# Optimization experiments

Measured on AMD Instinct MI355X. Metric: run time of the kernel, lower is better.

## Reference

```python
import jax, jax.numpy as jnp
import numpy as np


def conv3d(x, w, b):
    # x: [B,C,T,H,W], w: [O,I,3,3,3], padding=1, stride=1
    y = jax.lax.conv_general_dilated(
        x, w, window_strides=(1, 1, 1), padding=((1, 1), (1, 1), (1, 1)),
        dimension_numbers=('NCDHW', 'OIDHW', 'NCDHW'))
    return y + b[None, :, None, None, None]


def deform_conv3d(x, offsets, w, b):
    # Deformable 3D conv, kernel 3, pad 1, stride 1, no modulation mask.
    # offsets: [B, 81, T, H, W] -> [B, 27, 3(t,h,w), T, H, W]
    B, Cin, T, H, W = x.shape
    nk = 27
    off = offsets.reshape(B, nk, 3, T, H, W)
    r = jnp.arange(3, dtype=x.dtype) - 1.0  # kernel taps {-1,0,1}
    kt, kh, kw = jnp.meshgrid(r, r, r, indexing='ij')
    koff = jnp.stack([kt.ravel(), kh.ravel(), kw.ravel()], axis=-1)  # [27,3]
    bt = jnp.arange(T, dtype=x.dtype)[:, None, None]
    bh = jnp.arange(H, dtype=x.dtype)[None, :, None]
    bw = jnp.arange(W, dtype=x.dtype)[None, None, :]
    base = jnp.stack(jnp.broadcast_arrays(bt, bh, bw), axis=0)  # [3,T,H,W]
    pos = base[None, None] + koff[None, :, :, None, None, None] + off  # [B,27,3,T,H,W]
    pt, ph, pw = pos[:, :, 0], pos[:, :, 1], pos[:, :, 2]
    ft, fh, fw = jnp.floor(pt), jnp.floor(ph), jnp.floor(pw)
    at, ah, aw = pt - ft, ph - fh, pw - fw
    it, ih, iw = ft.astype(jnp.int32), fh.astype(jnp.int32), fw.astype(jnp.int32)
    N = T * H * W
    xf = x.reshape(B, Cin, N)
    gather = jax.vmap(lambda xb, lb: xb[:, lb])  # ([Cin,N],[27,N])->[Cin,27,N]
    acc = jnp.zeros((B, Cin, nk, N), dtype=x.dtype)
    # trilinear interpolation: accumulate 8 corners, zero outside bounds
    for dt in (0, 1):
        tti = it + dt
        wt = (1.0 - at) if dt == 0 else at
        vt = (tti >= 0) & (tti < T)
        tc = jnp.clip(tti, 0, T - 1)
        for dh in (0, 1):
            hhi = ih + dh
            wh = (1.0 - ah) if dh == 0 else ah
            vh = (hhi >= 0) & (hhi < H)
            hc = jnp.clip(hhi, 0, H - 1)
            for dw in (0, 1):
                wwi = iw + dw
                ww = (1.0 - aw) if dw == 0 else aw
                vw = (wwi >= 0) & (wwi < W)
                wc = jnp.clip(wwi, 0, W - 1)
                wgt = (wt * wh * ww) * (vt & vh & vw).astype(x.dtype)  # [B,27,T,H,W]
                lin = (tc * H + hc) * W + wc  # [B,27,T,H,W]
                g = gather(xf, lin.reshape(B, nk, N))  # [B,Cin,27,N]
                acc = acc + wgt.reshape(B, 1, nk, N) * g
    out = jnp.einsum('oik,bikn->bon', w.reshape(w.shape[0], Cin, nk), acc)
    out = out + b[None, :, None]
    return out.reshape(B, w.shape[0], T, H, W)


def setup_inputs() -> dict:
    key = jax.random.key(0)
    ks = jax.random.split(key, 12)
    B, Cin, Cout, mdim = 1, 256, 256, 256
    T, H, W = 8, 24, 24

    def winit(k, shape):
        fan_in = int(np.prod(shape[1:]))
        return jax.random.normal(k, shape, jnp.float32) / np.float32(np.sqrt(fan_in))

    return {
        'x': jax.random.normal(ks[0], (B, Cin, T, H, W), jnp.float32),
        'l1_w': winit(ks[1], (mdim, Cin, 3, 3, 3)),
        'l1_b': jnp.zeros((mdim,), jnp.float32),
        'l2_w': winit(ks[2], (mdim, mdim, 3, 3, 3)),
        'l2_b': jnp.zeros((mdim,), jnp.float32),
        'l3_w': winit(ks[3], (mdim, mdim, 3, 3, 3)),
        'l3_b': jnp.zeros((mdim,), jnp.float32),
        'def_w': winit(ks[4], (81, mdim, 3, 3, 3)) * 0.1,  # keep offsets small
        'def_b': jnp.zeros((81,), jnp.float32),
        'c3d_w': winit(ks[5], (Cout, Cin, 3, 3, 3)),
        'c3d_b': jnp.zeros((Cout,), jnp.float32),
    }


def reference(x, l1_w, l1_b, l2_w, l2_b, l3_w, l3_b, def_w, def_b, c3d_w, c3d_b):
    h = jax.nn.relu(conv3d(x, l1_w, l1_b))
    h = jax.nn.relu(conv3d(h, l2_w, l2_b))
    h = jax.nn.relu(conv3d(h, l3_w, l3_b))
    offsets = conv3d(h, def_w, def_b)  # [B,81,T,H,W]
    return deform_conv3d(x, offsets, c3d_w, c3d_b)
```

## Files before the change

kernel.cpp:

```cpp
#include <hip/hip_runtime.h>

#define TT 8
#define HH 24
#define WW 24
#define NN 4608
#define CIN 256
#define N3 6760
#define KDIM 6912
#define BK 64
#define KTILES 108
#define NSPLIT 9
#define KT_PER 12

typedef short short8 __attribute__((ext_vector_type(8)));
typedef short short4v __attribute__((ext_vector_type(4)));
typedef float f32x4  __attribute__((ext_vector_type(4)));
typedef int   i32x4  __attribute__((ext_vector_type(4)));
typedef unsigned int u32x4 __attribute__((ext_vector_type(4)));

#define MFMA16 __builtin_amdgcn_mfma_f32_16x16x32_bf16

__device__ __forceinline__ short f2bf(float f) {
    unsigned u = __float_as_uint(f);
    unsigned r = u + 0x7fffu + ((u >> 16) & 1u);
    return (short)(r >> 16);
}
__device__ __forceinline__ float bf2f(short s) {
    return __uint_as_float(((unsigned)(unsigned short)s) << 16);
}

__device__ __forceinline__ int n3_of(int n) {
    int t = n / (HH * WW), r = n % (HH * WW), h = r / WW, w = r % WW;
    return ((t + 1) * 26 + (h + 1)) * 26 + (w + 1);
}

__device__ __forceinline__ void gload16(const void* gsrc, void* lds) {
    __builtin_amdgcn_global_load_lds(
        (const __attribute__((address_space(1))) void*)gsrc,
        (__attribute__((address_space(3))) void*)lds, 16, 0, 0);
}

__global__ __launch_bounds__(256) void prep_k(
    const float* __restrict__ x,
    const float* __restrict__ w1, const float* __restrict__ w2,
    const float* __restrict__ w3, const float* __restrict__ wc,
    const float* __restrict__ wd,
    short* __restrict__ d1, short* __restrict__ d2,
    short* __restrict__ d3, short* __restrict__ dc, short* __restrict__ dd,
    short* __restrict__ xbf3, short* __restrict__ h1b)
{
    __shared__ char smem[27648];
    const int sel = blockIdx.y;

    if (sel < 5) {
        if (blockIdx.x >= 256) return;
        const int o = blockIdx.x, ci = threadIdx.x;
        const float* w; short* dst; int Cout = 256;
        if      (sel == 0) { w = w1; dst = d1; }
        else if (sel == 1) { w = w2; dst = d2; }
        else if (sel == 2) { w = w3; dst = d3; }
        else if (sel == 3) { w = wc; dst = dc; }
        else               { w = wd; dst = dd; Cout = 81; if (o >= 128) return; }
        float* buf = (float*)smem;
        if (o < Cout) {
            const float* src = w + (size_t)o * KDIM;
            #pragma unroll
            for (int j = 0; j < 27; ++j)
                buf[j * 256 + ci] = src[j * 256 + ci];
        }
        __syncthreads();
        const int row = o & 127, y = o >> 7;
        #pragma unroll
        for (int k = 0; k < 27; ++k) {
            int K = k * 256 + ci;
            int kt = K >> 6, kk = K & 63;
            int slot = (kk >> 3) ^ (row & 7), e = kk & 7;
            size_t idx = ((size_t)(y * KTILES + kt)) * 8192 + row * 64 + slot * 8 + e;
            float v = (o < Cout) ? buf[ci * 27 + k] : 0.f;
            dst[idx] = f2bf(v);
        }
    } else if (sel == 5) {
        float (*T)[65] = (float(*)[65])smem;
        const int bx = blockIdx.x;
        const int n0 = (bx % 72) * 64, ci0 = (bx / 72) * 64;
        const int lane = threadIdx.x & 63, wave = threadIdx.x >> 6;
        #pragma unroll
        for (int j = 0; j < 16; ++j) {
            int ci_l = wave * 16 + j;
            T[ci_l][lane] = x[(size_t)(ci0 + ci_l) * NN + n0 + lane];
        }
        __syncthreads();
        #pragma unroll
        for (int j = 0; j < 16; ++j) {
            int n_l = wave * 16 + j;
            xbf3[(size_t)n3_of(n0 + n_l) * 256 + ci0 + lane] = f2bf(T[lane][n_l]);
        }
    } else {
        const int tid = threadIdx.x;
        for (int r = blockIdx.x * 27; r < min((int)(blockIdx.x * 27 + 27), N3); ++r) {
            int t3 = r / 676, rem = r % 676, h3 = rem / 26, w3 = rem % 26;
            bool interior = (t3 >= 1 && t3 <= 8 && h3 >= 1 && h3 <= 24 && w3 >= 1 && w3 <= 24);
            if (!interior && tid < 128) {
                ((unsigned*)(xbf3 + (size_t)r * 256))[tid] = 0;
                ((unsigned*)(h1b  + (size_t)r * 256))[tid] = 0;
                ((unsigned*)(h1b + 1730560 + (size_t)r * 256))[tid] = 0;
                ((unsigned*)(h1b + 3461120 + (size_t)r * 256))[tid] = 0;
            }
        }
    }
}

__global__ __launch_bounds__(256) void sample_k(
    const short* __restrict__ xbf3, const short* __restrict__ Poff,
    const float* __restrict__ dfb, short* __restrict__ S)
{
    __shared__ char recs[64 * 64];
    const int k = blockIdx.y, n0 = blockIdx.x * 64;
    const int tid = threadIdx.x;

    if (tid < 64) {
        const int n = n0 + tid;
        const int t = n / (HH * WW), r = n % (HH * WW), h = r / WW, w2 = r % WW;
        const int ki = k / 9, kj = (k % 9) / 3, kl = k % 3;
        float po[3];
        #pragma unroll
        for (int d = 0; d < 3; ++d) {
            const int ch = k * 3 + d;
            float a = 0.f;
            #pragma unroll
            for (int s = 0; s < NSPLIT; ++s)
                a += bf2f(Poff[((size_t)(s * 128 + ch)) * NN + n]);
            po[d] = a + dfb[ch];
        }
        const float pt = (float)(t  + ki - 1) + po[0];
        const float ph = (float)(h  + kj - 1) + po[1];
        const float pw = (float)(w2 + kl - 1) + po[2];
        const float ft = floorf(pt), fh = floorf(ph), fw = floorf(pw);
        const float at = pt - ft, ah = ph - fh, aw = pw - fw;
        const int it = (int)ft, ih = (int)fh, iw = (int)fw;
        i32x4 idx[2]; f32x4 wgt[2];
        #pragma unroll
        for (int dt = 0; dt < 2; ++dt)
        #pragma unroll
        for (int dh = 0; dh < 2; ++dh)
        #pragma unroll
        for (int dw = 0; dw < 2; ++dw) {
            const int c = (dt * 2 + dh) * 2 + dw;
            const int ti = it + dt, hi = ih + dh, wi = iw + dw;
            const bool v = (ti >= 0) && (ti < TT) && (hi >= 0) && (hi < HH) && (wi >= 0) && (wi < WW);
            float wv = (dt ? at : 1.f - at) * (dh ? ah : 1.f - ah) * (dw ? aw : 1.f - aw);
            const int tc = min(max(ti, 0), TT - 1), hc = min(max(hi, 0), HH - 1), wc = min(max(wi, 0), WW - 1);
            const int r3 = ((tc + 1) * 26 + (hc + 1)) * 26 + (wc + 1);
            idx[c >> 2][c & 3] = r3 * 512;
            wgt[c >> 2][c & 3] = v ? wv : 0.f;
        }
        char* rec = &recs[tid * 64];
        *(i32x4*)(rec)      = idx[0];
        *(i32x4*)(rec + 16) = idx[1];
        *(f32x4*)(rec + 32) = wgt[0];
        *(f32x4*)(rec + 48) = wgt[1];
    }
    __syncthreads();

    const int lane = tid & 63, wave = tid >> 6;
    const int half = lane >> 5, lch = lane & 31;
    const char* xb = (const char*)xbf3 + lch * 16;
    short* Sk = S + (size_t)k * NN * 256 + lch * 8;

    for (int i = 0; i < 16; i += 4) {
        const int na = wave * 16 + i + half;
        const int nb = na + 2;
        const char* ra = &recs[na * 64];
        const char* rb = &recs[nb * 64];
        const i32x4 ia0 = *(const i32x4*)(ra);
        const i32x4 ia1 = *(const i32x4*)(ra + 16);
        const f32x4 wa0 = *(const f32x4*)(ra + 32);
        const f32x4 wa1 = *(const f32x4*)(ra + 48);
        const i32x4 ib0 = *(const i32x4*)(rb);
        const i32x4 ib1 = *(const i32x4*)(rb + 16);
        const f32x4 wb0 = *(const f32x4*)(rb + 32);
        const f32x4 wb1 = *(const f32x4*)(rb + 48);

        u32x4 ga[8], gb[8];
        #pragma unroll
        for (int c = 0; c < 4; ++c) {
            ga[c]     = *(const u32x4*)(xb + ia0[c]);
            ga[c + 4] = *(const u32x4*)(xb + ia1[c]);
            gb[c]     = *(const u32x4*)(xb + ib0[c]);
            gb[c + 4] = *(const u32x4*)(xb + ib1[c]);
        }

        float sa[8] = {}, sb[8] = {};
        #pragma unroll
        for (int c = 0; c < 8; ++c) {
            const float va = (c < 4) ? wa0[c & 3] : wa1[c & 3];
            const float vb = (c < 4) ? wb0[c & 3] : wb1[c & 3];
            #pragma unroll
            for (int j = 0; j < 4; ++j) {
                sa[2*j]   = fmaf(va, __uint_as_float(ga[c][j] << 16),         sa[2*j]);
                sa[2*j+1] = fmaf(va, __uint_as_float(ga[c][j] & 0xffff0000u), sa[2*j+1]);
                sb[2*j]   = fmaf(vb, __uint_as_float(gb[c][j] << 16),         sb[2*j]);
                sb[2*j+1] = fmaf(vb, __uint_as_float(gb[c][j] & 0xffff0000u), sb[2*j+1]);
            }
        }
        short8 oa, ob;
        #pragma unroll
        for (int m = 0; m < 8; ++m) { oa[m] = f2bf(sa[m]); ob[m] = f2bf(sb[m]); }
        *(short8*)(Sk + (size_t)(n0 + na) * 256) = oa;
        *(short8*)(Sk + (size_t)(n0 + nb) * 256) = ob;
    }
}

template<int CP>
__global__ __launch_bounds__(256, 3) void gemm_conv_sk(
    const short* __restrict__ src,
    const short* __restrict__ wrb_sw,
    short* __restrict__ P)
{
    __shared__ short Ap[8192];
    __shared__ short Bw[8192];
    const int tid = threadIdx.x;
    const int l = tid & 63, w = tid >> 6;
    const int n0 = blockIdx.x * 128, co0 = blockIdx.y * 128, split = blockIdx.z;
    const int wr = w >> 1, wc = w & 1;
    const int lm = l & 15, lq = l >> 4;
    const int rswz = (lm & 7) << 3;
    const int kt0 = split * KT_PER;

    const int colA = 8 * ((l & 7) ^ ((l >> 3) & 7));
    int r3[4];
    #pragma unroll
    for (int j = 0; j < 4; ++j)
        r3[j] = n3_of(n0 + w * 32 + j * 8 + (l >> 3));
    const short* bbase = wrb_sw + ((size_t)blockIdx.y * KTILES) * 8192 + (w * 4) * 512 + l * 8;

    f32x4 acc[4][4] = {};

    for (int i = 0; i < KT_PER; ++i) {
        const int kt = kt0 + i;
        const int k = kt >> 2, ci0 = (kt & 3) * 64;
        const int dt = k / 9 - 1, dh = (k % 9) / 3 - 1, dw = k % 3 - 1;
        const int d3 = (dt * 26 + dh) * 26 + dw;
        #pragma unroll
        for (int j = 0; j < 4; ++j)
            gload16(src + (size_t)(r3[j] + d3) * 256 + ci0 + colA, &Ap[(w * 4 + j) * 512]);
        const short* b = bbase + (size_t)kt * 8192;
        #pragma unroll
        for (int j = 0; j < 4; ++j)
            gload16(b + j * 512, &Bw[(w * 4 + j) * 512]);
        __syncthreads();
        #pragma unroll
        for (int ks = 0; ks < 2; ++ks) {
            const int c = (ks * 32 + lq * 8) ^ rswz;
            short8 a[4], bf[4];
            #pragma unroll
            for (int m = 0; m < 4; ++m)
                a[m] = *(const short8*)&Ap[(wr * 64 + m * 16 + lm) * 64 + c];
            #pragma unroll
            for (int nb = 0; nb < 4; ++nb)
                bf[nb] = *(const short8*)&Bw[(wc * 64 + nb * 16 + lm) * 64 + c];
            #pragma unroll
            for (int m = 0; m < 4; ++m)
            #pragma unroll
            for (int nb = 0; nb < 4; ++nb)
                acc[m][nb] = MFMA16(a[m], bf[nb], acc[m][nb], 0, 0, 0);
        }
        __syncthreads();
    }
    #pragma unroll
    for (int m = 0; m < 4; ++m)
    #pragma unroll
    for (int nb = 0; nb < 4; ++nb) {
        int co = co0 + wc * 64 + nb * 16 + lm;
        int n = n0 + wr * 64 + m * 16 + lq * 4;
        short4v o;
        #pragma unroll
        for (int j = 0; j < 4; ++j) o[j] = f2bf(acc[m][nb][j]);
        *(short4v*)(P + ((size_t)split * CP + co) * NN + n) = o;
    }
}

__global__ __launch_bounds__(256, 3) void gemm_deform_sk(
    const short* __restrict__ S,
    const short* __restrict__ wrb_sw,
    short* __restrict__ P)
{
    __shared__ short Ap[8192];
    __shared__ short Bw[8192];
    const int tid = threadIdx.x;
    const int l = tid & 63, w = tid >> 6;
    const int n0 = blockIdx.x * 128, co0 = blockIdx.y * 128, split = blockIdx.z;
    const int wr = w >> 1, wc = w & 1;
    const int lm = l & 15, lq = l >> 4;
    const int rswz = (lm & 7) << 3;
    const int kt0 = split * KT_PER;

    const int colA = 8 * ((l & 7) ^ ((l >> 3) & 7));
    int rA[4];
    #pragma unroll
    for (int j = 0; j < 4; ++j)
        rA[j] = n0 + w * 32 + j * 8 + (l >> 3);
    const short* bbase = wrb_sw + ((size_t)blockIdx.y * KTILES) * 8192 + (w * 4) * 512 + l * 8;

    f32x4 acc[4][4] = {};

    for (int i = 0; i < KT_PER; ++i) {
        const int kt = kt0 + i;
        const int k = kt >> 2, ci0 = (kt & 3) * 64;
        #pragma unroll
        for (int j = 0; j < 4; ++j)
            gload16(S + ((size_t)k * NN + rA[j]) * 256 + ci0 + colA, &Ap[(w * 4 + j) * 512]);
        const short* b = bbase + (size_t)kt * 8192;
        #pragma unroll
        for (int j = 0; j < 4; ++j)
            gload16(b + j * 512, &Bw[(w * 4 + j) * 512]);
        __syncthreads();
        #pragma unroll
        for (int ks = 0; ks < 2; ++ks) {
            const int c = (ks * 32 + lq * 8) ^ rswz;
            short8 a[4], bf[4];
            #pragma unroll
            for (int m = 0; m < 4; ++m)
                a[m] = *(const short8*)&Ap[(wr * 64 + m * 16 + lm) * 64 + c];
            #pragma unroll
            for (int nb = 0; nb < 4; ++nb)
                bf[nb] = *(const short8*)&Bw[(wc * 64 + nb * 16 + lm) * 64 + c];
            #pragma unroll
            for (int m = 0; m < 4; ++m)
            #pragma unroll
            for (int nb = 0; nb < 4; ++nb)
                acc[m][nb] = MFMA16(a[m], bf[nb], acc[m][nb], 0, 0, 0);
        }
        __syncthreads();
    }
    #pragma unroll
    for (int m = 0; m < 4; ++m)
    #pragma unroll
    for (int nb = 0; nb < 4; ++nb) {
        int co = co0 + wc * 64 + nb * 16 + lm;
        int n = n0 + wr * 64 + m * 16 + lq * 4;
        short4v o;
        #pragma unroll
        for (int j = 0; j < 4; ++j) o[j] = f2bf(acc[m][nb][j]);
        *(short4v*)(P + ((size_t)split * 256 + co) * NN + n) = o;
    }
}

template<bool RELU>
__global__ __launch_bounds__(256) void reduce_k(
    const short* __restrict__ P, const float* __restrict__ bias,
    float* __restrict__ dst, int Cout, int CP)
{
    int id = blockIdx.x * 256 + threadIdx.x;
    int total = Cout * (NN / 4);
    if (id >= total) return;
    int co = id / (NN / 4), n4 = id - co * (NN / 4);
    const short* p0 = P + ((size_t)co) * NN + n4 * 4;
    float v[4] = {};
    #pragma unroll
    for (int s = 0; s < NSPLIT; ++s) {
        short4v u = *(const short4v*)(p0 + (size_t)s * CP * NN);
        #pragma unroll
        for (int q = 0; q < 4; ++q) v[q] += bf2f(u[q]);
    }
    float bv = bias[co];
    f32x4 o;
    #pragma unroll
    for (int q = 0; q < 4; ++q) {
        float f = v[q] + bv;
        if (RELU) f = fmaxf(f, 0.f);
        o[q] = f;
    }
    *(f32x4*)(dst + (size_t)co * NN + n4 * 4) = o;
}

__global__ __launch_bounds__(256) void reduce_bf3(
    const short* __restrict__ P, const float* __restrict__ bias,
    short* __restrict__ dst)
{
    __shared__ float T[64][65];
    const int lane = threadIdx.x & 63, wave = threadIdx.x >> 6;
    const int n0 = blockIdx.x * 64, co0 = blockIdx.y * 64;
    #pragma unroll
    for (int j = 0; j < 16; ++j) {
        int co_l = wave * 16 + j, co = co0 + co_l;
        const short* p0 = P + (size_t)co * NN + n0 + lane;
        float a = 0.f;
        #pragma unroll
        for (int s = 0; s < NSPLIT; ++s) a += bf2f(p0[(size_t)s * 256 * NN]);
        T[co_l][lane] = fmaxf(a + bias[co], 0.f);
    }
    __syncthreads();
    #pragma unroll
    for (int j = 0; j < 16; ++j) {
        int n_l = wave * 16 + j;
        dst[(size_t)n3_of(n0 + n_l) * 256 + co0 + lane] = f2bf(T[lane][n_l]);
    }
}

extern "C" void kernel_launch(void* const* d_in, const int* in_sizes, int n_in,
                              void* d_out, int out_size, void* d_ws, size_t ws_size,
                              hipStream_t stream)
{
    const float* x   = (const float*)d_in[0];
    const float* l1w = (const float*)d_in[1];
    const float* l1b = (const float*)d_in[2];
    const float* l2w = (const float*)d_in[3];
    const float* l2b = (const float*)d_in[4];
    const float* l3w = (const float*)d_in[5];
    const float* l3b = (const float*)d_in[6];
    const float* dfw = (const float*)d_in[7];
    const float* dfb = (const float*)d_in[8];
    const float* c3w = (const float*)d_in[9];
    const float* c3b = (const float*)d_in[10];
    float* out = (float*)d_out;

    char* base = (char*)d_ws;
    short* S    = (short*)base;
    short* h1b  = (short*)(base);
    short* wrb1 = (short*)(base + 10383360);
    short* wrb2 = (short*)(base + 13922304);
    short* wrb3 = (short*)(base + 17461248);
    short* wrbd = (short*)(base + 21000192);
    short* h2b  = (short*)(base + 3461120);
    short* h3b  = (short*)(base + 6922240);
    char* q = base + 63700992;
    short* xbf3 = (short*)q; q += 3461120;
    short* wrbc = (short*)q; q += 3538944;
    short* P    = (short*)q;

    const dim3 blk(256);
    prep_k<<<dim3(288, 7), blk, 0, stream>>>(x, l1w, l2w, l3w, c3w, dfw,
                                             wrb1, wrb2, wrb3, wrbc, wrbd,
                                             xbf3, h1b);

    const int rg256 = (256 * (NN / 4) + 255) / 256;

    gemm_conv_sk<256><<<dim3(36, 2, NSPLIT), blk, 0, stream>>>(xbf3, wrb1, P);
    reduce_bf3       <<<dim3(72, 4),         blk, 0, stream>>>(P, l1b, h1b);
    gemm_conv_sk<256><<<dim3(36, 2, NSPLIT), blk, 0, stream>>>(h1b, wrb2, P);
    reduce_bf3       <<<dim3(72, 4),         blk, 0, stream>>>(P, l2b, h2b);
    gemm_conv_sk<256><<<dim3(36, 2, NSPLIT), blk, 0, stream>>>(h2b, wrb3, P);
    reduce_bf3       <<<dim3(72, 4),         blk, 0, stream>>>(P, l3b, h3b);
    gemm_conv_sk<128><<<dim3(36, 1, NSPLIT), blk, 0, stream>>>(h3b, wrbd, P);

    sample_k<<<dim3(72, 27), blk, 0, stream>>>(xbf3, P, dfb, S);
    gemm_deform_sk<<<dim3(36, 2, NSPLIT), blk, 0, stream>>>(S, wrbc, P);
    reduce_k<false><<<dim3(rg256), blk, 0, stream>>>(P, c3b, out, 256, 256);
}
```

Measured before the change: 195.6 us.

## Double-buffer LDS tiles in split-K conv and deform GEMMs to overlap loads

Measured after the change: 218.5 us, median of 2. 11.7% more time.

```diff
diff --git a/kernel.cpp b/kernel.cpp
--- a/kernel.cpp
+++ b/kernel.cpp
@@ -212,13 +212,13 @@
 }
 
 template<int CP>
-__global__ __launch_bounds__(256, 3) void gemm_conv_sk(
+__global__ __launch_bounds__(256, 2) void gemm_conv_sk(
     const short* __restrict__ src,
     const short* __restrict__ wrb_sw,
     short* __restrict__ P)
 {
-    __shared__ short Ap[8192];
-    __shared__ short Bw[8192];
+    __shared__ short Ap[2][8192];
+    __shared__ short Bw[2][8192];
     const int tid = threadIdx.x;
     const int l = tid & 63, w = tid >> 6;
     const int n0 = blockIdx.x * 128, co0 = blockIdx.y * 128, split = blockIdx.z;
@@ -234,38 +234,48 @@
         r3[j] = n3_of(n0 + w * 32 + j * 8 + (l >> 3));
     const short* bbase = wrb_sw + ((size_t)blockIdx.y * KTILES) * 8192 + (w * 4) * 512 + l * 8;
 
-    f32x4 acc[4][4] = {};
-
-    for (int i = 0; i < KT_PER; ++i) {
-        const int kt = kt0 + i;
+    auto stage = [&](int buf, int kt) {
         const int k = kt >> 2, ci0 = (kt & 3) * 64;
         const int dt = k / 9 - 1, dh = (k % 9) / 3 - 1, dw = k % 3 - 1;
         const int d3 = (dt * 26 + dh) * 26 + dw;
         #pragma unroll
         for (int j = 0; j < 4; ++j)
-            gload16(src + (size_t)(r3[j] + d3) * 256 + ci0 + colA, &Ap[(w * 4 + j) * 512]);
+            gload16(src + (size_t)(r3[j] + d3) * 256 + ci0 + colA, &Ap[buf][(w * 4 + j) * 512]);
         const short* b = bbase + (size_t)kt * 8192;
         #pragma unroll
         for (int j = 0; j < 4; ++j)
-            gload16(b + j * 512, &Bw[(w * 4 + j) * 512]);
-        __syncthreads();
+            gload16(b + j * 512, &Bw[buf][(w * 4 + j) * 512]);
+    };
+
+    f32x4 acc[4][4] = {};
+    int cur = 0;
+    stage(0, kt0);
+
+    for (int i = 0; i < KT_PER; ++i) {
+        if (i + 1 < KT_PER) {
+            stage(cur ^ 1, kt0 + i + 1);
+            asm volatile("s_waitcnt vmcnt(8)\n\ts_barrier" ::: "memory");
+        } else {
+            asm volatile("s_waitcnt vmcnt(0)\n\ts_barrier" ::: "memory");
+        }
         #pragma unroll
         for (int ks = 0; ks < 2; ++ks) {
             const int c = (ks * 32 + lq * 8) ^ rswz;
             short8 a[4], bf[4];
             #pragma unroll
             for (int m = 0; m < 4; ++m)
-                a[m] = *(const short8*)&Ap[(wr * 64 + m * 16 + lm) * 64 + c];
+                a[m] = *(const short8*)&Ap[cur][(wr * 64 + m * 16 + lm) * 64 + c];
             #pragma unroll
             for (int nb = 0; nb < 4; ++nb)
-                bf[nb] = *(const short8*)&Bw[(wc * 64 + nb * 16 + lm) * 64 + c];
+                bf[nb] = *(const short8*)&Bw[cur][(wc * 64 + nb * 16 + lm) * 64 + c];
             #pragma unroll
             for (int m = 0; m < 4; ++m)
             #pragma unroll
             for (int nb = 0; nb < 4; ++nb)
                 acc[m][nb] = MFMA16(a[m], bf[nb], acc[m][nb], 0, 0, 0);
         }
-        __syncthreads();
+        asm volatile("s_barrier" ::: "memory");
+        cur ^= 1;
     }
     #pragma unroll
     for (int m = 0; m < 4; ++m)
@@ -280,13 +290,13 @@
     }
 }
 
-__global__ __launch_bounds__(256, 3) void gemm_deform_sk(
+__global__ __launch_bounds__(256, 2) void gemm_deform_sk(
     const short* __restrict__ S,
     const short* __restrict__ wrb_sw,
     short* __restrict__ P)
 {
-    __shared__ short Ap[8192];
-    __shared__ short Bw[8192];
+    __shared__ short Ap[2][8192];
+    __shared__ short Bw[2][8192];
     const int tid = threadIdx.x;
     const int l = tid & 63, w = tid >> 6;
     const int n0 = blockIdx.x * 128, co0 = blockIdx.y * 128, split = blockIdx.z;
@@ -302,36 +312,46 @@
         rA[j] = n0 + w * 32 + j * 8 + (l >> 3);
     const short* bbase = wrb_sw + ((size_t)blockIdx.y * KTILES) * 8192 + (w * 4) * 512 + l * 8;
 
+    auto stage = [&](int buf, int kt) {
+        const int k = kt >> 2, ci0 = (kt & 3) * 64;
+        #pragma unroll
+        for (int j = 0; j < 4; ++j)
+            gload16(S + ((size_t)k * NN + rA[j]) * 256 + ci0 + colA, &Ap[buf][(w * 4 + j) * 512]);
+        const short* b = bbase + (size_t)kt * 8192;
+        #pragma unroll
+        for (int j = 0; j < 4; ++j)
+            gload16(b + j * 512, &Bw[buf][(w * 4 + j) * 512]);
+    };
+
     f32x4 acc[4][4] = {};
+    int cur = 0;
+    stage(0, kt0);
 
     for (int i = 0; i < KT_PER; ++i) {
-        const int kt = kt0 + i;
-        const int k = kt >> 2, ci0 = (kt & 3) * 64;
-        #pragma unroll
-        for (int j = 0; j < 4; ++j)
-            gload16(S + ((size_t)k * NN + rA[j]) * 256 + ci0 + colA, &Ap[(w * 4 + j) * 512]);
-        const short* b = bbase + (size_t)kt * 8192;
-        #pragma unroll
-        for (int j = 0; j < 4; ++j)
-            gload16(b + j * 512, &Bw[(w * 4 + j) * 512]);
-        __syncthreads();
+        if (i + 1 < KT_PER) {
+            stage(cur ^ 1, kt0 + i + 1);
+            asm volatile("s_waitcnt vmcnt(8)\n\ts_barrier" ::: "memory");
+        } else {
+            asm volatile("s_waitcnt vmcnt(0)\n\ts_barrier" ::: "memory");
+        }
         #pragma unroll
         for (int ks = 0; ks < 2; ++ks) {
             const int c = (ks * 32 + lq * 8) ^ rswz;
             short8 a[4], bf[4];
             #pragma unroll
             for (int m = 0; m < 4; ++m)
-                a[m] = *(const short8*)&Ap[(wr * 64 + m * 16 + lm) * 64 + c];
+                a[m] = *(const short8*)&Ap[cur][(wr * 64 + m * 16 + lm) * 64 + c];
             #pragma unroll
             for (int nb = 0; nb < 4; ++nb)
-                bf[nb] = *(const short8*)&Bw[(wc * 64 + nb * 16 + lm) * 64 + c];
+                bf[nb] = *(const short8*)&Bw[cur][(wc * 64 + nb * 16 + lm) * 64 + c];
             #pragma unroll
             for (int m = 0; m < 4; ++m)
             #pragma unroll
             for (int nb = 0; nb < 4; ++nb)
                 acc[m][nb] = MFMA16(a[m], bf[nb], acc[m][nb], 0, 0, 0);
         }
-        __syncthreads();
+        asm volatile("s_barrier" ::: "memory");
+        cur ^= 1;
     }
     #pragma unroll
     for (int m = 0; m < 4; ++m)
```
